# Optimization experiments

Measured on AMD Instinct MI355X. Metric: run time of the kernel, lower is better.

Reference implementation:

```python
import jax, jax.numpy as jnp
import numpy as np

N_EMBD = 2048
NUM_GROUPS = 8
EXPERTS_PER_GROUP = 8
ROUTER_TEMPERATURE = 1.0
N_TOKENS = 16384


def setup_inputs() -> dict:
    key = jax.random.key(0)
    kx, kg, ke = jax.random.split(key, 3)
    x = jax.random.normal(kx, (N_TOKENS, N_EMBD), dtype=jnp.float32)
    # nn.Linear(in, out, bias=False) stores weight as [out, in]; kaiming-uniform-ish scale
    bound = 1.0 / np.sqrt(N_EMBD)
    group_gate_w = jax.random.uniform(kg, (NUM_GROUPS, N_EMBD), dtype=jnp.float32,
                                      minval=-bound, maxval=bound)
    expert_gate_w = jax.random.uniform(ke, (NUM_GROUPS * EXPERTS_PER_GROUP, N_EMBD),
                                       dtype=jnp.float32, minval=-bound, maxval=bound)
    return {"x": x, "group_gate_w": group_gate_w, "expert_gate_w": expert_gate_w}


def reference(x, group_gate_w, expert_gate_w):
    N = x.shape[0]
    G = NUM_GROUPS
    E_g = EXPERTS_PER_GROUP
    inv_temp = 1.0 / ROUTER_TEMPERATURE

    # Level 1: group routing
    group_logits = jnp.einsum('nd,gd->ng', x, group_gate_w)            # [N, G]
    group_probs = jax.nn.softmax(group_logits * inv_temp, axis=-1)     # [N, G]
    group_mask = group_probs >= (1.0 / G)                              # [N, G]

    # Level 2: expert routing within each group
    expert_logits = jnp.einsum('nd,ed->ne', x, expert_gate_w)          # [N, G*E_g]
    expert_logits = expert_logits.reshape(N, G, E_g)
    expert_probs = jax.nn.softmax(expert_logits * inv_temp, axis=-1)   # [N, G, E_g]
    expert_mask = expert_probs >= (1.0 / E_g)                          # [N, G, E_g]

    valid_mask_3d = group_mask[:, :, None] & expert_mask               # [N, G, E_g]
    selected_weights_3d = (group_probs[:, :, None] * expert_probs) * valid_mask_3d.astype(x.dtype)

    valid_mask = valid_mask_3d.reshape(N, G * E_g)
    selected_weights = selected_weights_3d.reshape(N, G * E_g)
    weight_sum = jnp.clip(jnp.sum(selected_weights, axis=-1, keepdims=True), 1e-9, None)
    normalized_weights = selected_weights / weight_sum
    return (valid_mask, normalized_weights)
```

## Files before the change

### kernel.cpp

```cpp
#include <hip/hip_runtime.h>
#include <hip/hip_bf16.h>


#define NT 16384
#define NE 2048

__global__ __launch_bounds__(512, 2)
void router(const float* __restrict__ x, const float* __restrict__ gw,
            const float* __restrict__ ew, float* __restrict__ out)
{
    __shared__ __align__(16) float sm[26624];

    const int tid = threadIdx.x;
    const int w   = tid >> 6;
    const int l   = tid & 63;
    const int row = l & 7;
    const int col = l >> 3;
    const int t0  = blockIdx.x * 64;

    float* xs = sm + w * 1024;
    float* es = sm + 8192 + w * 1024;
    float* gs = sm + 16384 + w * 128;

    const int k0 = w * 256;

    float accE[8][8];
    float accG[8];
    #pragma unroll
    for (int i = 0; i < 8; ++i) {
        accG[i] = 0.f;
        #pragma unroll
        for (int j = 0; j < 8; ++j) accE[i][j] = 0.f;
    }

    const float* xg = x  + (size_t)(t0 + l) * NE + k0;
    const float* eg = ew + (size_t)l        * NE + k0;
    const float* gp = gw + (size_t)(l >> 2) * NE + k0 + (l & 3)*4;

    float4 rx0 = *(const float4*)(xg + 0),  rx1 = *(const float4*)(xg + 4);
    float4 rx2 = *(const float4*)(xg + 8),  rx3 = *(const float4*)(xg + 12);
    float4 re0 = *(const float4*)(eg + 0),  re1 = *(const float4*)(eg + 4);
    float4 re2 = *(const float4*)(eg + 8),  re3 = *(const float4*)(eg + 12);
    float4 rg;
    if (l < 32) rg = *(const float4*)(gp);

    for (int it = 0; it < 16; ++it) {
        xs[ 0*64+l]=rx0.x; xs[ 1*64+l]=rx0.y; xs[ 2*64+l]=rx0.z; xs[ 3*64+l]=rx0.w;
        xs[ 4*64+l]=rx1.x; xs[ 5*64+l]=rx1.y; xs[ 6*64+l]=rx1.z; xs[ 7*64+l]=rx1.w;
        xs[ 8*64+l]=rx2.x; xs[ 9*64+l]=rx2.y; xs[10*64+l]=rx2.z; xs[11*64+l]=rx2.w;
        xs[12*64+l]=rx3.x; xs[13*64+l]=rx3.y; xs[14*64+l]=rx3.z; xs[15*64+l]=rx3.w;
        es[ 0*64+l]=re0.x; es[ 1*64+l]=re0.y; es[ 2*64+l]=re0.z; es[ 3*64+l]=re0.w;
        es[ 4*64+l]=re1.x; es[ 5*64+l]=re1.y; es[ 6*64+l]=re1.z; es[ 7*64+l]=re1.w;
        es[ 8*64+l]=re2.x; es[ 9*64+l]=re2.y; es[10*64+l]=re2.z; es[11*64+l]=re2.w;
        es[12*64+l]=re3.x; es[13*64+l]=re3.y; es[14*64+l]=re3.z; es[15*64+l]=re3.w;
        if (l < 32) {
            const int g = l >> 2, q = l & 3;
            gs[(q*4+0)*8+g]=rg.x; gs[(q*4+1)*8+g]=rg.y;
            gs[(q*4+2)*8+g]=rg.z; gs[(q*4+3)*8+g]=rg.w;
        }

        if (it + 1 < 16) {
            const int kb = (it + 1) * 16;
            rx0 = *(const float4*)(xg + kb + 0);  rx1 = *(const float4*)(xg + kb + 4);
            rx2 = *(const float4*)(xg + kb + 8);  rx3 = *(const float4*)(xg + kb + 12);
            re0 = *(const float4*)(eg + kb + 0);  re1 = *(const float4*)(eg + kb + 4);
            re2 = *(const float4*)(eg + kb + 8);  re3 = *(const float4*)(eg + kb + 12);
            if (l < 32) rg = *(const float4*)(gp + kb);
        }

        #pragma unroll 4
        for (int kk = 0; kk < 16; ++kk) {
            float4 a = *(const float4*)&xs[kk*64 + col*8];
            float4 b = *(const float4*)&xs[kk*64 + col*8 + 4];
            float4 c = *(const float4*)&es[kk*64 + row*8];
            float4 d = *(const float4*)&es[kk*64 + row*8 + 4];
            float  g = gs[kk*8 + row];
            float xv[8] = {a.x,a.y,a.z,a.w,b.x,b.y,b.z,b.w};
            float wv[8] = {c.x,c.y,c.z,c.w,d.x,d.y,d.z,d.w};
            #pragma unroll
            for (int i = 0; i < 8; ++i) {
                #pragma unroll
                for (int j = 0; j < 8; ++j)
                    accE[i][j] = fmaf(xv[i], wv[j], accE[i][j]);
                accG[i] = fmaf(xv[i], g, accG[i]);
            }
        }
    }

    __syncthreads();

    #define WRITE_C(r) { float* C = sm + (r)*4608;                                   \
        _Pragma("unroll") for (int i = 0; i < 8; ++i) { const int t = col*8 + i;     \
            *(float4*)&C[t*72 + row*8]   = make_float4(accE[i][0],accE[i][1],accE[i][2],accE[i][3]); \
            *(float4*)&C[t*72 + row*8+4] = make_float4(accE[i][4],accE[i][5],accE[i][6],accE[i][7]); \
            C[t*72 + 64 + row] = accG[i]; } }
    #define ADD_C(r) { const float* C = sm + (r)*4608;                               \
        _Pragma("unroll") for (int i = 0; i < 8; ++i) { const int t = col*8 + i;     \
            float4 a_ = *(const float4*)&C[t*72 + row*8];                            \
            float4 b_ = *(const float4*)&C[t*72 + row*8+4];                          \
            accE[i][0]+=a_.x; accE[i][1]+=a_.y; accE[i][2]+=a_.z; accE[i][3]+=a_.w;  \
            accE[i][4]+=b_.x; accE[i][5]+=b_.y; accE[i][6]+=b_.z; accE[i][7]+=b_.w;  \
            accG[i] += C[t*72 + 64 + row]; } }

    if (w >= 4) WRITE_C(w - 4);
    __syncthreads();
    if (w < 4)  ADD_C(w);
    __syncthreads();
    if (w == 2 || w == 3) WRITE_C(w - 2);
    __syncthreads();
    if (w < 2)  ADD_C(w);
    __syncthreads();
    if (w == 1) WRITE_C(0);
    __syncthreads();
    if (w == 0) { ADD_C(0); WRITE_C(0); }
    __syncthreads();

    if (tid < 64) {
        const float* lg = sm + tid * 72;
        float* M = sm + 18432 + tid * 64;
        float* W = sm + 22528 + tid * 64;

        float gpb[8];
        float gmax = lg[64];
        #pragma unroll
        for (int g = 1; g < 8; ++g) gmax = fmaxf(gmax, lg[64 + g]);
        float gsum = 0.f;
        #pragma unroll
        for (int g = 0; g < 8; ++g) { gpb[g] = __expf(lg[64 + g] - gmax); gsum += gpb[g]; }
        const float ginv = 1.f / gsum;

        float sel[64];
        float wsum = 0.f;
        #pragma unroll
        for (int g = 0; g < 8; ++g) {
            const float gp_ = gpb[g] * ginv;
            float emax = lg[g * 8];
            #pragma unroll
            for (int j = 1; j < 8; ++j) emax = fmaxf(emax, lg[g * 8 + j]);
            float ep[8]; float esum = 0.f;
            #pragma unroll
            for (int j = 0; j < 8; ++j) { ep[j] = __expf(lg[g * 8 + j] - emax); esum += ep[j]; }
            const float einv = 1.f / esum;
            const bool gm = gp_ >= 0.125f;
            #pragma unroll
            for (int j = 0; j < 8; ++j) {
                const float pe = ep[j] * einv;
                const bool v = gm && (pe >= 0.125f);
                const float ww = v ? gp_ * pe : 0.f;
                M[g * 8 + j] = v ? 1.f : 0.f;
                sel[g * 8 + j] = ww;
                wsum += ww;
            }
        }
        const float inv = 1.f / fmaxf(wsum, 1e-9f);
        #pragma unroll
        for (int e = 0; e < 64; ++e) W[e] = sel[e] * inv;
    }
    __syncthreads();

    const float4* M4 = (const float4*)(sm + 18432);
    const float4* W4 = (const float4*)(sm + 22528);
    float4* o0 = (float4*)(out + (size_t)t0 * 64);
    float4* o1 = (float4*)(out + (size_t)NT * 64 + (size_t)t0 * 64);
    o0[tid]       = M4[tid];
    o0[tid + 512] = M4[tid + 512];
    o1[tid]       = W4[tid];
    o1[tid + 512] = W4[tid + 512];

    #undef WRITE_C
    #undef ADD_C
}

extern "C" void kernel_launch(void* const* d_in, const int* in_sizes, int n_in,
                              void* d_out, int out_size, void* d_ws, size_t ws_size,
                              hipStream_t stream) {
    const float* x  = (const float*)d_in[0];
    const float* gw = (const float*)d_in[1];
    const float* ew = (const float*)d_in[2];
    float* out = (float*)d_out;
    (void)d_ws; (void)ws_size;

    router<<<dim3(NT / 64), dim3(512), 0, stream>>>(x, gw, ew, out);
}
```

Before: 228.1 us.

## Compute router logits with split-fp16 MFMA and double-buffered LDS staging

Replaces the scalar FP32 FMA GEMM with MFMA 16x16x32 f16 instructions, splitting each fp32 operand into high and scaled-low fp16 halves so three MFMAs approximate fp32 precision. Inputs are staged in 128-wide K chunks through a double-buffered LDS layout, and the cross-wave reduction is simplified to a single two-way split-K step. The goal is to move the dot products onto matrix cores, but it uses about 159KB of LDS, which may cap occupancy at one block per CU despite launch_bounds requesting 2, and the split-fp16 scheme may change mask decisions near the thresholds.

```diff
diff --git a/kernel.cpp b/kernel.cpp
--- a/kernel.cpp
+++ b/kernel.cpp
@@ -4,121 +4,169 @@
 
 #define NT 16384
 #define NE 2048
+#define KC 128
+#define NCHUNK 16
+
+#define QS    272
+#define PL    1088
+#define FP    2208
+#define XB    44160
+#define BUFSZ 79488
+#define LDS_BYTES 158976
+
+typedef _Float16 v8h __attribute__((ext_vector_type(8)));
+typedef float    v4f __attribute__((ext_vector_type(4)));
 
 __global__ __launch_bounds__(512, 2)
 void router(const float* __restrict__ x, const float* __restrict__ gw,
             const float* __restrict__ ew, float* __restrict__ out)
 {
-    __shared__ __align__(16) float sm[26624];
-
-    const int tid = threadIdx.x;
-    const int w   = tid >> 6;
-    const int l   = tid & 63;
-    const int row = l & 7;
-    const int col = l >> 3;
-    const int t0  = blockIdx.x * 64;
-
-    float* xs = sm + w * 1024;
-    float* es = sm + 8192 + w * 1024;
-    float* gs = sm + 16384 + w * 128;
-
-    const int k0 = w * 256;
-
-    float accE[8][8];
-    float accG[8];
-    #pragma unroll
-    for (int i = 0; i < 8; ++i) {
-        accG[i] = 0.f;
-        #pragma unroll
-        for (int j = 0; j < 8; ++j) accE[i][j] = 0.f;
-    }
-
-    const float* xg = x  + (size_t)(t0 + l) * NE + k0;
-    const float* eg = ew + (size_t)l        * NE + k0;
-    const float* gp = gw + (size_t)(l >> 2) * NE + k0 + (l & 3)*4;
-
-    float4 rx0 = *(const float4*)(xg + 0),  rx1 = *(const float4*)(xg + 4);
-    float4 rx2 = *(const float4*)(xg + 8),  rx3 = *(const float4*)(xg + 12);
-    float4 re0 = *(const float4*)(eg + 0),  re1 = *(const float4*)(eg + 4);
-    float4 re2 = *(const float4*)(eg + 8),  re3 = *(const float4*)(eg + 12);
-    float4 rg;
-    if (l < 32) rg = *(const float4*)(gp);
-
-    for (int it = 0; it < 16; ++it) {
-        xs[ 0*64+l]=rx0.x; xs[ 1*64+l]=rx0.y; xs[ 2*64+l]=rx0.z; xs[ 3*64+l]=rx0.w;
-        xs[ 4*64+l]=rx1.x; xs[ 5*64+l]=rx1.y; xs[ 6*64+l]=rx1.z; xs[ 7*64+l]=rx1.w;
-        xs[ 8*64+l]=rx2.x; xs[ 9*64+l]=rx2.y; xs[10*64+l]=rx2.z; xs[11*64+l]=rx2.w;
-        xs[12*64+l]=rx3.x; xs[13*64+l]=rx3.y; xs[14*64+l]=rx3.z; xs[15*64+l]=rx3.w;
-        es[ 0*64+l]=re0.x; es[ 1*64+l]=re0.y; es[ 2*64+l]=re0.z; es[ 3*64+l]=re0.w;
-        es[ 4*64+l]=re1.x; es[ 5*64+l]=re1.y; es[ 6*64+l]=re1.z; es[ 7*64+l]=re1.w;
-        es[ 8*64+l]=re2.x; es[ 9*64+l]=re2.y; es[10*64+l]=re2.z; es[11*64+l]=re2.w;
-        es[12*64+l]=re3.x; es[13*64+l]=re3.y; es[14*64+l]=re3.z; es[15*64+l]=re3.w;
-        if (l < 32) {
-            const int g = l >> 2, q = l & 3;
-            gs[(q*4+0)*8+g]=rg.x; gs[(q*4+1)*8+g]=rg.y;
-            gs[(q*4+2)*8+g]=rg.z; gs[(q*4+3)*8+g]=rg.w;
-        }
-
-        if (it + 1 < 16) {
-            const int kb = (it + 1) * 16;
-            rx0 = *(const float4*)(xg + kb + 0);  rx1 = *(const float4*)(xg + kb + 4);
-            rx2 = *(const float4*)(xg + kb + 8);  rx3 = *(const float4*)(xg + kb + 12);
-            re0 = *(const float4*)(eg + kb + 0);  re1 = *(const float4*)(eg + kb + 4);
-            re2 = *(const float4*)(eg + kb + 8);  re3 = *(const float4*)(eg + kb + 12);
-            if (l < 32) rg = *(const float4*)(gp + kb);
-        }
-
-        #pragma unroll 4
-        for (int kk = 0; kk < 16; ++kk) {
-            float4 a = *(const float4*)&xs[kk*64 + col*8];
-            float4 b = *(const float4*)&xs[kk*64 + col*8 + 4];
-            float4 c = *(const float4*)&es[kk*64 + row*8];
-            float4 d = *(const float4*)&es[kk*64 + row*8 + 4];
-            float  g = gs[kk*8 + row];
-            float xv[8] = {a.x,a.y,a.z,a.w,b.x,b.y,b.z,b.w};
-            float wv[8] = {c.x,c.y,c.z,c.w,d.x,d.y,d.z,d.w};
-            #pragma unroll
-            for (int i = 0; i < 8; ++i) {
+    __shared__ __align__(16) char sm[LDS_BYTES];
+    const int tid  = threadIdx.x;
+    const int lane = tid & 63;
+    const int w    = tid >> 6;
+    const int t0   = blockIdx.x * 64;
+
+    const float* wsrc[3]; int who[3]; int wmode[3];
+    #pragma unroll
+    for (int i = 0; i < 3; ++i) {
+        int s = tid + i * 512;
+        if (s >= 1280) { wmode[i] = 0; wsrc[i] = ew; who[i] = 0; continue; }
+        int gate = s >> 4, kslot = s & 15;
+        int ks = kslot >> 2, q = kslot & 3;
+        who[i] = ((gate >> 4) * 4 + ks) * FP + q * QS + (gate & 15) * 16;
+        if (gate < 64)      { wmode[i] = 2; wsrc[i] = ew + (size_t)gate * NE + kslot * 8; }
+        else if (gate < 72) { wmode[i] = 2; wsrc[i] = gw + (size_t)(gate - 64) * NE + kslot * 8; }
+        else                { wmode[i] = 1; wsrc[i] = ew; }
+    }
+    const float* xsrc[2]; int xho[2];
+    #pragma unroll
+    for (int i = 0; i < 2; ++i) {
+        int s = tid + i * 512;
+        int token = s >> 4, kslot = s & 15;
+        int ks = kslot >> 2, q = kslot & 3;
+        xho[i] = XB + ((token >> 4) * 4 + ks) * FP + q * QS + (token & 15) * 16;
+        xsrc[i] = x + (size_t)(t0 + token) * NE + kslot * 8;
+    }
+
+    float4 wr[3][2], xr[2][2];
+
+    auto stage_load = [&](int c) {
+        const int kc = c * KC;
+        #pragma unroll
+        for (int i = 0; i < 3; ++i) {
+            if (wmode[i] == 2) {
+                wr[i][0] = *(const float4*)(wsrc[i] + kc);
+                wr[i][1] = *(const float4*)(wsrc[i] + kc + 4);
+            } else {
+                wr[i][0] = make_float4(0.f, 0.f, 0.f, 0.f);
+                wr[i][1] = make_float4(0.f, 0.f, 0.f, 0.f);
+            }
+        }
+        #pragma unroll
+        for (int i = 0; i < 2; ++i) {
+            xr[i][0] = *(const float4*)(xsrc[i] + kc);
+            xr[i][1] = *(const float4*)(xsrc[i] + kc + 4);
+        }
+    };
+
+    auto split8 = [](const float4& a, const float4& b, v8h& h, v8h& l) {
+        float v[8] = {a.x, a.y, a.z, a.w, b.x, b.y, b.z, b.w};
+        #pragma unroll
+        for (int j = 0; j < 8; ++j) {
+            _Float16 hh = (_Float16)v[j];
+            h[j] = hh;
+            l[j] = (_Float16)((v[j] - (float)hh) * 2048.0f);
+        }
+    };
+
+    auto stage_commit = [&](int buf) {
+        const int bb = buf * BUFSZ;
+        #pragma unroll
+        for (int i = 0; i < 3; ++i) {
+            if (wmode[i] == 0) continue;
+            v8h h, l;
+            split8(wr[i][0], wr[i][1], h, l);
+            *(v8h*)(sm + bb + who[i])      = h;
+            *(v8h*)(sm + bb + who[i] + PL) = l;
+        }
+        #pragma unroll
+        for (int i = 0; i < 2; ++i) {
+            v8h h, l;
+            split8(xr[i][0], xr[i][1], h, l);
+            *(v8h*)(sm + bb + xho[i])      = h;
+            *(v8h*)(sm + bb + xho[i] + PL) = l;
+        }
+    };
+
+    const int tt = w & 3, s2 = w >> 2;
+    v4f accHH[5], accC[5];
+    #pragma unroll
+    for (int g = 0; g < 5; ++g) { accHH[g] = (v4f)(0.f); accC[g] = (v4f)(0.f); }
+    const int rdo = (lane >> 4) * QS + (lane & 15) * 16;
+
+    stage_load(0);
+    stage_commit(0);
+    for (int c = 0; c < NCHUNK; ++c) {
+        if (c + 1 < NCHUNK) stage_load(c + 1);
+        __syncthreads();
+        {
+            const int bb = (c & 1) * BUFSZ;
+            #pragma unroll
+            for (int ksl = 0; ksl < 2; ++ksl) {
+                const int ks = s2 * 2 + ksl;
+                const char* xb = sm + bb + XB + (tt * 4 + ks) * FP + rdo;
+                v8h Bh = *(const v8h*)xb;
+                v8h Bl = *(const v8h*)(xb + PL);
                 #pragma unroll
-                for (int j = 0; j < 8; ++j)
-                    accE[i][j] = fmaf(xv[i], wv[j], accE[i][j]);
-                accG[i] = fmaf(xv[i], g, accG[i]);
-            }
-        }
-    }
-
-    __syncthreads();
-
-    #define WRITE_C(r) { float* C = sm + (r)*4608;                                   \
-        _Pragma("unroll") for (int i = 0; i < 8; ++i) { const int t = col*8 + i;     \
-            *(float4*)&C[t*72 + row*8]   = make_float4(accE[i][0],accE[i][1],accE[i][2],accE[i][3]); \
-            *(float4*)&C[t*72 + row*8+4] = make_float4(accE[i][4],accE[i][5],accE[i][6],accE[i][7]); \
-            C[t*72 + 64 + row] = accG[i]; } }
-    #define ADD_C(r) { const float* C = sm + (r)*4608;                               \
-        _Pragma("unroll") for (int i = 0; i < 8; ++i) { const int t = col*8 + i;     \
-            float4 a_ = *(const float4*)&C[t*72 + row*8];                            \
-            float4 b_ = *(const float4*)&C[t*72 + row*8+4];                          \
-            accE[i][0]+=a_.x; accE[i][1]+=a_.y; accE[i][2]+=a_.z; accE[i][3]+=a_.w;  \
-            accE[i][4]+=b_.x; accE[i][5]+=b_.y; accE[i][6]+=b_.z; accE[i][7]+=b_.w;  \
-            accG[i] += C[t*72 + 64 + row]; } }
-
-    if (w >= 4) WRITE_C(w - 4);
-    __syncthreads();
-    if (w < 4)  ADD_C(w);
-    __syncthreads();
-    if (w == 2 || w == 3) WRITE_C(w - 2);
-    __syncthreads();
-    if (w < 2)  ADD_C(w);
-    __syncthreads();
-    if (w == 1) WRITE_C(0);
-    __syncthreads();
-    if (w == 0) { ADD_C(0); WRITE_C(0); }
+                for (int g = 0; g < 5; ++g) {
+                    const char* wb = sm + bb + (g * 4 + ks) * FP + rdo;
+                    v8h Ah = *(const v8h*)wb;
+                    v8h Al = *(const v8h*)(wb + PL);
+                    accHH[g] = __builtin_amdgcn_mfma_f32_16x16x32_f16(Ah, Bh, accHH[g], 0, 0, 0);
+                    accC[g]  = __builtin_amdgcn_mfma_f32_16x16x32_f16(Ah, Bl, accC[g], 0, 0, 0);
+                    accC[g]  = __builtin_amdgcn_mfma_f32_16x16x32_f16(Al, Bh, accC[g], 0, 0, 0);
+                }
+            }
+        }
+        if (c + 1 < NCHUNK) stage_commit((c + 1) & 1);
+    }
+    __syncthreads();
+
+    float part[5][4];
+    #pragma unroll
+    for (int g = 0; g < 5; ++g)
+        #pragma unroll
+        for (int r = 0; r < 4; ++r)
+            part[g][r] = accHH[g][r] + accC[g][r] * (1.0f / 2048.0f);
+
+    float* red = (float*)sm;
+    if (w >= 4) {
+        #pragma unroll
+        for (int g = 0; g < 5; ++g)
+            #pragma unroll
+            for (int r = 0; r < 4; ++r)
+                red[((tt * 5 + g) * 4 + r) * 64 + lane] = part[g][r];
+    }
+    __syncthreads();
+    float* la = (float*)(sm + 24576);
+    if (w < 4) {
+        #pragma unroll
+        for (int g = 0; g < 5; ++g)
+            #pragma unroll
+            for (int r = 0; r < 4; ++r) {
+                float v = part[g][r] + red[((tt * 5 + g) * 4 + r) * 64 + lane];
+                int gate  = g * 16 + (lane >> 4) * 4 + r;
+                int token = tt * 16 + (lane & 15);
+                la[token * 80 + gate] = v;
+            }
+    }
     __syncthreads();
 
     if (tid < 64) {
-        const float* lg = sm + tid * 72;
-        float* M = sm + 18432 + tid * 64;
-        float* W = sm + 22528 + tid * 64;
+        const float* lg = la + tid * 80;
+        float* M = (float*)(sm + 45056) + tid * 64;
+        float* W = (float*)(sm + 61440) + tid * 64;
 
         float gpb[8];
         float gmax = lg[64];
@@ -158,17 +206,14 @@
     }
     __syncthreads();
 
-    const float4* M4 = (const float4*)(sm + 18432);
-    const float4* W4 = (const float4*)(sm + 22528);
+    const float4* M4 = (const float4*)(sm + 45056);
+    const float4* W4 = (const float4*)(sm + 61440);
     float4* o0 = (float4*)(out + (size_t)t0 * 64);
     float4* o1 = (float4*)(out + (size_t)NT * 64 + (size_t)t0 * 64);
     o0[tid]       = M4[tid];
     o0[tid + 512] = M4[tid + 512];
     o1[tid]       = W4[tid];
     o1[tid + 512] = W4[tid + 512];
-
-    #undef WRITE_C
-    #undef ADD_C
 }
 
 extern "C" void kernel_launch(void* const* d_in, const int* in_sizes, int n_in,
```

After: 201.0 us. -11.8%, faster.
